# Optimization experiments

Measured on AMD Instinct MI355X. Metric: run time of the kernel, lower is better.

## Reference

```python
import jax, jax.numpy as jnp
import numpy as np

B, S, E = 2, 2048, 1024
D_ATTN, H = 1024, 16
HD = D_ATTN // H
SCALE = 1.0 / np.sqrt(D_ATTN)
ROPE_BASE = 10000.0


def setup_inputs() -> dict:
    key = jax.random.key(0)
    ks = jax.random.split(key, 7)
    def w(k, shape, scale):
        return jax.random.normal(k, shape, dtype=jnp.float32) * scale
    return {
        "q": w(ks[0], (B, S, E), 1.0),
        "k": w(ks[1], (B, S, E), 1.0),
        "v": w(ks[2], (B, S, E), 1.0),
        "Wq": w(ks[3], (D_ATTN, E), E ** -0.5),
        "Wk": w(ks[4], (D_ATTN, E), E ** -0.5),
        "Wv": w(ks[5], (D_ATTN, E), E ** -0.5),
        "Wo": w(ks[6], (E, D_ATTN), D_ATTN ** -0.5),
    }


def _rope(x):
    # x: [B, H, S, HD]; interleaved-pair rotary embedding over the seq axis
    s, d = x.shape[2], x.shape[3]
    half = d // 2
    inv_freq = 1.0 / (ROPE_BASE ** (jnp.arange(half, dtype=jnp.float32) * 2.0 / d))
    ang = jnp.arange(s, dtype=jnp.float32)[:, None] * inv_freq[None, :]  # [S, half]
    cos, sin = jnp.cos(ang), jnp.sin(ang)
    xr = x.reshape(x.shape[:-1] + (half, 2))
    x0, x1 = xr[..., 0], xr[..., 1]
    o0 = x0 * cos - x1 * sin
    o1 = x0 * sin + x1 * cos
    return jnp.stack([o0, o1], axis=-1).reshape(x.shape)


def reference(q, k, v, Wq, Wk, Wv, Wo):
    # linear projections (nn.Linear with weight [out, in]): y = x @ W^T
    qh = (q @ Wq.T).reshape(B, S, H, HD).transpose(0, 2, 1, 3)  # [B,H,S,HD]
    kh = (k @ Wk.T).reshape(B, S, H, HD).transpose(0, 2, 1, 3)
    vh = (v @ Wv.T).reshape(B, S, H, HD).transpose(0, 2, 1, 3)
    qh = _rope(qh)
    kh = _rope(kh)
    # shifted-causal mask: disallow j >= i (diagonal masked), except (0,0) allowed
    i = jnp.arange(S)[:, None]
    j = jnp.arange(S)[None, :]
    masked = j >= i                              # triu incl. diagonal
    masked = masked.at[0, 0].set(False)          # keep (0,0) so row 0 isn't all -inf
    scores = jnp.einsum("bhsd,bhtd->bhst", qh, kh) * SCALE
    scores = jnp.where(masked, -jnp.inf, scores)
    probs = jax.nn.softmax(scores, axis=-1)      # dropout omitted (eval mode)
    ctx = jnp.einsum("bhst,bhtd->bhsd", probs, vh)
    ctx = ctx.transpose(0, 2, 1, 3).reshape(B, S, D_ATTN)
    return ctx @ Wo.T
```

## Files before the change

### kernel.cpp

```cpp
#include <hip/hip_runtime.h>
#include <hip/hip_bf16.h>

#define BATCH 2
#define SEQ   2048
#define EMB   1024
#define DATTN 1024
#define NH    16
#define HD    64
#define MM    (BATCH*SEQ)
#define SCALE 0.03125f
#define MINIT -1.0e30f
#define ROPE_COEF 0.41524101186f

using bf16x8 = __attribute__((ext_vector_type(8))) short;
using f32x4  = __attribute__((ext_vector_type(4))) float;

__device__ inline short f2bf(float x) {
    __hip_bfloat16 b = __float2bfloat16(x);
    return *reinterpret_cast<short*>(&b);
}

__device__ inline void gl_lds16(const short* g, short* l) {
    __builtin_amdgcn_global_load_lds(
        (const __attribute__((address_space(1))) unsigned int*)g,
        (__attribute__((address_space(3))) unsigned int*)l, 16, 0, 0);
}

__global__ __launch_bounds__(256)
void cvt_all(const float* __restrict__ q, const float* __restrict__ k,
             const float* __restrict__ v,
             const float* __restrict__ Wq, const float* __restrict__ Wk,
             const float* __restrict__ Wv, const float* __restrict__ Wo,
             short* __restrict__ dst)
{
    const long QKV = (long)MM * EMB;
    const long WSZ = (long)DATTN * EMB;
    const long i = ((long)blockIdx.x * 256 + threadIdx.x) * 4;
    const float* s;
    long off;
    if (i < 3 * QKV) {
        const int seg = (int)(i / QKV);
        off = i - (long)seg * QKV;
        s = (seg == 0) ? q : (seg == 1) ? k : v;
    } else {
        const long j = i - 3 * QKV;
        const int seg = (int)(j / WSZ);
        off = j - (long)seg * WSZ;
        s = (seg == 0) ? Wq : (seg == 1) ? Wk : (seg == 2) ? Wv : Wo;
    }
    float4 x = *(const float4*)(s + off);
    short4 y;
    y.x = f2bf(x.x); y.y = f2bf(x.y); y.z = f2bf(x.z); y.w = f2bf(x.w);
    *(short4*)(dst + i) = y;
}

__device__ inline void stage_tile64(const short* g, short* lds, int tid) {
    #pragma unroll
    for (int c = 0; c < 4; ++c) {
        const int cc   = c * 256 + tid;
        const int row  = cc >> 3;
        const int slot = cc & 7;
        const int ssl  = slot ^ (row & 7);
        gl_lds16(g + (long)row * EMB + ssl * 8, lds + ((cc & ~63) << 3));
    }
}

__device__ inline void stage_tile64h(const short* g, short* lds, int tid) {
    #pragma unroll
    for (int c = 0; c < 2; ++c) {
        const int cc   = c * 256 + tid;
        const int row  = cc >> 3;
        const int ssl  = (cc & 7) ^ (row & 7);
        gl_lds16(g + (long)row * EMB + ssl * 8, lds + ((cc & ~63) << 3));
    }
}

__global__ __launch_bounds__(256)
void gemm_proj_bf16(const short* __restrict__ qb, const short* __restrict__ kb,
                    const short* __restrict__ vb,
                    const short* __restrict__ wqb, const short* __restrict__ wkb,
                    const short* __restrict__ wvb,
                    short* __restrict__ Qb, short* __restrict__ Kb,
                    short* __restrict__ Vtb)
{
    const short* A; const short* B;
    if (blockIdx.z == 0)      { A = qb; B = wqb; }
    else if (blockIdx.z == 1) { A = kb; B = wkb; }
    else                      { A = vb; B = wvb; }
    const bool isv = (blockIdx.z == 2);

    __shared__ short sA[128 * 64];
    __shared__ short sB[128 * 64];

    const int tid  = threadIdx.x;
    const int wave = tid >> 6, lane = tid & 63;
    const int quad = lane >> 4, l16 = lane & 15;
    const int wm = (wave >> 1) * 64, wn = (wave & 1) * 64;
    const long m0 = (long)blockIdx.x * 128, n0 = (long)blockIdx.y * 128;
    const int rsw = l16 & 7;

    f32x4 acc[4][4];
    #pragma unroll
    for (int i = 0; i < 4; ++i)
        #pragma unroll
        for (int j = 0; j < 4; ++j) acc[i][j] = (f32x4){0.f, 0.f, 0.f, 0.f};

    for (int kt = 0; kt < EMB; kt += 64) {
        __syncthreads();
        stage_tile64(A + m0 * EMB + kt, sA, tid);
        stage_tile64(B + n0 * EMB + kt, sB, tid);
        __syncthreads();

        #pragma unroll
        for (int kk = 0; kk < 2; ++kk) {
            bf16x8 af[4], bfr[4];
            #pragma unroll
            for (int rt = 0; rt < 4; ++rt)
                af[rt] = *(const bf16x8*)&sA[(wm + rt * 16 + l16) * 64
                         + (((kk << 2) | quad) ^ rsw) * 8];
            #pragma unroll
            for (int ct = 0; ct < 4; ++ct)
                bfr[ct] = *(const bf16x8*)&sB[(wn + ct * 16 + l16) * 64
                          + (((kk << 2) | quad) ^ rsw) * 8];
            if (isv) {
                #pragma unroll
                for (int i = 0; i < 4; ++i)
                    #pragma unroll
                    for (int j = 0; j < 4; ++j)
                        acc[i][j] = __builtin_amdgcn_mfma_f32_16x16x32_bf16(
                            af[i], bfr[j], acc[i][j], 0, 0, 0);
            } else {
                #pragma unroll
                for (int i = 0; i < 4; ++i)
                    #pragma unroll
                    for (int j = 0; j < 4; ++j)
                        acc[i][j] = __builtin_amdgcn_mfma_f32_16x16x32_bf16(
                            bfr[i], af[j], acc[i][j], 0, 0, 0);
            }
        }
    }

    if (!isv) {
        short* C = (blockIdx.z == 0) ? Qb : Kb;
        const float scl = (blockIdx.z == 0) ? SCALE : 1.0f;
        #pragma unroll
        for (int i = 0; i < 4; ++i) {
            const int d0  = (int)(n0) + wn + i * 16 + quad * 4;
            const int hh  = d0 >> 6, dd0 = d0 & (HD - 1);
            const float invf0 = exp2f(-ROPE_COEF * (float)(dd0 >> 1));
            const float invf1 = exp2f(-ROPE_COEF * (float)((dd0 >> 1) + 1));
            #pragma unroll
            for (int j = 0; j < 4; ++j) {
                const int tok = (int)(m0) + wm + j * 16 + l16;
                const int bb = tok >> 11, ss = tok & (SEQ - 1);
                float s0, c0, s1, c1;
                __sincosf((float)ss * invf0, &s0, &c0);
                __sincosf((float)ss * invf1, &s1, &c1);
                const f32x4 x = acc[i][j];
                short4 o4;
                o4.x = f2bf((x[0] * c0 - x[1] * s0) * scl);
                o4.y = f2bf((x[0] * s0 + x[1] * c0) * scl);
                o4.z = f2bf((x[2] * c1 - x[3] * s1) * scl);
                o4.w = f2bf((x[2] * s1 + x[3] * c1) * scl);
                *(short4*)&C[(((long)(bb * NH + hh)) << 17)
                             + ((long)ss << 6) + dd0] = o4;
            }
        }
    } else {
        #pragma unroll
        for (int rt = 0; rt < 4; ++rt) {
            #pragma unroll
            for (int ct = 0; ct < 4; ++ct) {
                const long row0 = m0 + wm + rt * 16 + quad * 4;
                const long col  = n0 + wn + ct * 16 + l16;
                const int bb = (int)(row0 >> 11), ss = (int)(row0 & (SEQ - 1));
                const int hh = (int)(col >> 6),   dd = (int)(col & (HD - 1));
                short4 s4;
                s4.x = f2bf(acc[rt][ct][0]); s4.y = f2bf(acc[rt][ct][1]);
                s4.z = f2bf(acc[rt][ct][2]); s4.w = f2bf(acc[rt][ct][3]);
                *(short4*)&Vtb[(((long)(bb * NH + hh)) << 17) + ((long)dd << 11) + ss] = s4;
            }
        }
    }
}

__global__ __launch_bounds__(256)
void gemm_out_bf16(const short* __restrict__ Ab, const short* __restrict__ Bb,
                   float* __restrict__ C)
{
    __shared__ short sA[128 * 64];
    __shared__ short sB[64 * 64];

    const int tid  = threadIdx.x;
    const int wave = tid >> 6, lane = tid & 63;
    const int quad = lane >> 4, l16 = lane & 15;
    const int wm = (wave >> 1) * 64, wn = (wave & 1) * 32;
    const long m0 = (long)blockIdx.x * 128, n0 = (long)blockIdx.y * 64;
    const int rsw = l16 & 7;

    f32x4 acc[4][2];
    #pragma unroll
    for (int i = 0; i < 4; ++i)
        #pragma unroll
        for (int j = 0; j < 2; ++j) acc[i][j] = (f32x4){0.f, 0.f, 0.f, 0.f};

    for (int kt = 0; kt < DATTN; kt += 64) {
        __syncthreads();
        stage_tile64(Ab + m0 * DATTN + kt, sA, tid);
        stage_tile64h(Bb + n0 * DATTN + kt, sB, tid);
        __syncthreads();

        #pragma unroll
        for (int kk = 0; kk < 2; ++kk) {
            bf16x8 af[4], bfr[2];
            #pragma unroll
            for (int rt = 0; rt < 4; ++rt)
                af[rt] = *(const bf16x8*)&sA[(wm + rt * 16 + l16) * 64
                         + (((kk << 2) | quad) ^ rsw) * 8];
            #pragma unroll
            for (int ct = 0; ct < 2; ++ct)
                bfr[ct] = *(const bf16x8*)&sB[(wn + ct * 16 + l16) * 64
                          + (((kk << 2) | quad) ^ rsw) * 8];
            #pragma unroll
            for (int rt = 0; rt < 4; ++rt)
                #pragma unroll
                for (int ct = 0; ct < 2; ++ct)
                    acc[rt][ct] = __builtin_amdgcn_mfma_f32_16x16x32_bf16(
                        af[rt], bfr[ct], acc[rt][ct], 0, 0, 0);
        }
    }

    #pragma unroll
    for (int rt = 0; rt < 4; ++rt) {
        #pragma unroll
        for (int ct = 0; ct < 2; ++ct) {
            #pragma unroll
            for (int reg = 0; reg < 4; ++reg) {
                const long row = m0 + wm + rt * 16 + quad * 4 + reg;
                const long col = n0 + wn + ct * 16 + l16;
                C[row * EMB + col] = acc[rt][ct][reg];
            }
        }
    }
}

#define KLD 64
#define PLD 72

__device__ inline void stage_kv64(const short* __restrict__ Kb,
                                  const short* __restrict__ Vtb,
                                  long base, int jb2,
                                  short* skp, short* svp,
                                  int tid, int wave)
{
    #pragma unroll
    for (int c = 0; c < 2; ++c) {
        const int cc  = c * 256 + tid;
        const int row = cc >> 3;
        const int sch = (cc & 7) ^ (row & 7);
        short* dk = skp + ((c * 256 + (tid & ~63)) << 3) - ((tid & ~63) << 3)
                        + (((c * 256 + tid) & ~63) - (c * 256 + tid - (tid & 63)) ) ;
        (void)dk;
        gl_lds16(Kb + base + (long)(jb2 + row) * HD + sch * 8,
                 skp + ((c * 256 + wave * 64) << 3));
        gl_lds16(Vtb + base + ((long)row << 11) + jb2 + sch * 8,
                 svp + ((c * 256 + wave * 64) << 3));
    }
}

__global__ __launch_bounds__(256, 3)
void flash_attn_mfma(const short* __restrict__ Qb,
                     const short* __restrict__ Kb,
                     const short* __restrict__ Vtb,
                     short* __restrict__ ctx)
{
    const int id  = blockIdx.x;
    const int hi  = id >> 8;
    const int idx = id & 255;
    const int r   = idx & 7;
    const int s5  = idx >> 3;
    const int pi  = s5 & 3;
    const int ts8 = s5 >> 2;
    const int p   = r + 8 * pi;
    const int b   = p >> 4, h = p & 15;
    const int t   = hi ? ts8 : (15 - ts8);

    const int tid = threadIdx.x;
    const int wave = tid >> 6, lane = tid & 63;
    const int quad = lane >> 4, l16 = lane & 15;
    const int r0 = t * 128;

    __shared__ short sk[2][64 * KLD];
    __shared__ short sv[2][64 * KLD];
    __shared__ short sp[4][32 * PLD];

    const long base = ((long)(b * NH + h)) << 17;

    const int iq0 = r0 + wave * 32 + l16;
    const int iq1 = iq0 + 16;
    const int dtile = 2 * t + (wave >> 1);
    const int rsw = l16 & 7;

    bf16x8 qf0[2], qf1[2];
    #pragma unroll
    for (int tt = 0; tt < 2; ++tt) {
        qf0[tt] = *(const bf16x8*)(Qb + base + (long)iq0 * HD + tt * 32 + quad * 8);
        qf1[tt] = *(const bf16x8*)(Qb + base + (long)iq1 * HD + tt * 32 + quad * 8);
    }

    f32x4 acc0[4], acc1[4];
    #pragma unroll
    for (int ct = 0; ct < 4; ++ct) {
        acc0[ct] = (f32x4){0.f, 0.f, 0.f, 0.f};
        acc1[ct] = (f32x4){0.f, 0.f, 0.f, 0.f};
    }
    float m0 = MINIT, l0 = 0.f;
    float m1 = MINIT, l1 = 0.f;

    const int J = 2 * t + 2;

    stage_kv64(Kb, Vtb, base, 0, sk[0], sv[0], tid, wave);

    #pragma unroll 1
    for (int j2 = 0; j2 < J; ++j2) {
        const int pb = j2 & 1;
        asm volatile("s_waitcnt vmcnt(0)" ::: "memory");
        __builtin_amdgcn_s_barrier();
        if (j2 + 1 < J)
            stage_kv64(Kb, Vtb, base, (j2 + 1) * 64,
                       sk[pb ^ 1], sv[pb ^ 1], tid, wave);

        if (j2 <= dtile) {
            const int jb2 = j2 * 64;
            const short* skh = sk[pb];
            const short* svh = sv[pb];

            f32x4 s0[4], s1[4];
            __builtin_amdgcn_s_setprio(1);
            #pragma unroll
            for (int ct = 0; ct < 4; ++ct) {
                const int rr16 = (ct * 16 + l16) * KLD;
                bf16x8 k0 = *(const bf16x8*)&skh[rr16 + ((quad ^ rsw) << 3)];
                bf16x8 k1 = *(const bf16x8*)&skh[rr16 + (((4 + quad) ^ rsw) << 3)];
                f32x4 z0 = (f32x4){0.f, 0.f, 0.f, 0.f};
                z0 = __builtin_amdgcn_mfma_f32_16x16x32_bf16(k0, qf0[0], z0, 0, 0, 0);
                z0 = __builtin_amdgcn_mfma_f32_16x16x32_bf16(k1, qf0[1], z0, 0, 0, 0);
                s0[ct] = z0;
                f32x4 z1 = (f32x4){0.f, 0.f, 0.f, 0.f};
                z1 = __builtin_amdgcn_mfma_f32_16x16x32_bf16(k0, qf1[0], z1, 0, 0, 0);
                z1 = __builtin_amdgcn_mfma_f32_16x16x32_bf16(k1, qf1[1], z1, 0, 0, 0);
                s1[ct] = z1;
            }
            __builtin_amdgcn_s_setprio(0);

            if (j2 == dtile) {
                #pragma unroll
                for (int ct = 0; ct < 4; ++ct)
                    #pragma unroll
                    for (int rr = 0; rr < 4; ++rr) {
                        const int j = jb2 + ct * 16 + quad * 4 + rr;
                        if (!((j < iq0) || (iq0 == 0 && j == 0)))
                            s0[ct][rr] = -INFINITY;
                        if (!(j < iq1))
                            s1[ct][rr] = -INFINITY;
                    }
            }

            float mx0 = MINIT;
            #pragma unroll
            for (int ct = 0; ct < 4; ++ct)
                #pragma unroll
                for (int rr = 0; rr < 4; ++rr) mx0 = fmaxf(mx0, s0[ct][rr]);
            mx0 = fmaxf(mx0, __shfl_xor(mx0, 16, 64));
            mx0 = fmaxf(mx0, __shfl_xor(mx0, 32, 64));
            const float mn0 = fmaxf(m0, mx0);
            const float a0 = __expf(m0 - mn0);
            m0 = mn0;
            float ss0 = 0.f;
            #pragma unroll
            for (int ct = 0; ct < 4; ++ct)
                #pragma unroll
                for (int rr = 0; rr < 4; ++rr) {
                    const float e = __expf(s0[ct][rr] - mn0);
                    s0[ct][rr] = e;
                    ss0 += e;
                }
            ss0 += __shfl_xor(ss0, 16, 64);
            ss0 += __shfl_xor(ss0, 32, 64);
            l0 = l0 * a0 + ss0;

            float mx1 = MINIT;
            #pragma unroll
            for (int ct = 0; ct < 4; ++ct)
                #pragma unroll
                for (int rr = 0; rr < 4; ++rr) mx1 = fmaxf(mx1, s1[ct][rr]);
            mx1 = fmaxf(mx1, __shfl_xor(mx1, 16, 64));
            mx1 = fmaxf(mx1, __shfl_xor(mx1, 32, 64));
            const float mn1 = fmaxf(m1, mx1);
            const float a1 = __expf(m1 - mn1);
            m1 = mn1;
            float ss1 = 0.f;
            #pragma unroll
            for (int ct = 0; ct < 4; ++ct)
                #pragma unroll
                for (int rr = 0; rr < 4; ++rr) {
                    const float e = __expf(s1[ct][rr] - mn1);
                    s1[ct][rr] = e;
                    ss1 += e;
                }
            ss1 += __shfl_xor(ss1, 16, 64);
            ss1 += __shfl_xor(ss1, 32, 64);
            l1 = l1 * a1 + ss1;

            short* pw0 = sp[wave];
            short* pw1 = sp[wave] + 16 * PLD;
            #pragma unroll
            for (int ct = 0; ct < 4; ++ct) {
                short4 p4;
                p4.x = f2bf(s0[ct][0]); p4.y = f2bf(s0[ct][1]);
                p4.z = f2bf(s0[ct][2]); p4.w = f2bf(s0[ct][3]);
                *(short4*)&pw0[l16 * PLD + ct * 16 + quad * 4] = p4;
                short4 q4;
                q4.x = f2bf(s1[ct][0]); q4.y = f2bf(s1[ct][1]);
                q4.z = f2bf(s1[ct][2]); q4.w = f2bf(s1[ct][3]);
                *(short4*)&pw1[l16 * PLD + ct * 16 + quad * 4] = q4;
            }

            #pragma unroll
            for (int ct = 0; ct < 4; ++ct)
                #pragma unroll
                for (int rr = 0; rr < 4; ++rr) {
                    acc0[ct][rr] *= a0;
                    acc1[ct][rr] *= a1;
                }

            bf16x8 pf00 = *(const bf16x8*)&pw0[l16 * PLD + quad * 8];
            bf16x8 pf01 = *(const bf16x8*)&pw0[l16 * PLD + 32 + quad * 8];
            bf16x8 pf10 = *(const bf16x8*)&pw1[l16 * PLD + quad * 8];
            bf16x8 pf11 = *(const bf16x8*)&pw1[l16 * PLD + 32 + quad * 8];

            __builtin_amdgcn_s_setprio(1);
            #pragma unroll
            for (int ct = 0; ct < 4; ++ct) {
                const int rr16 = (ct * 16 + l16) * KLD;
                bf16x8 v0 = *(const bf16x8*)&svh[rr16 + ((quad ^ rsw) << 3)];
                bf16x8 v1 = *(const bf16x8*)&svh[rr16 + (((4 + quad) ^ rsw) << 3)];
                acc0[ct] = __builtin_amdgcn_mfma_f32_16x16x32_bf16(
                    v0, pf00, acc0[ct], 0, 0, 0);
                acc0[ct] = __builtin_amdgcn_mfma_f32_16x16x32_bf16(
                    v1, pf01, acc0[ct], 0, 0, 0);
                acc1[ct] = __builtin_amdgcn_mfma_f32_16x16x32_bf16(
                    v0, pf10, acc1[ct], 0, 0, 0);
                acc1[ct] = __builtin_amdgcn_mfma_f32_16x16x32_bf16(
                    v1, pf11, acc1[ct], 0, 0, 0);
            }
            __builtin_amdgcn_s_setprio(0);
        }
    }

    {
        const float inv0 = 1.f / l0;
        short* orow = ctx + (long)(b * SEQ + iq0) * DATTN + h * HD;
        #pragma unroll
        for (int ct = 0; ct < 4; ++ct) {
            short4 o4;
            o4.x = f2bf(acc0[ct][0] * inv0);
            o4.y = f2bf(acc0[ct][1] * inv0);
            o4.z = f2bf(acc0[ct][2] * inv0);
            o4.w = f2bf(acc0[ct][3] * inv0);
            *(short4*)&orow[ct * 16 + quad * 4] = o4;
        }
    }
    {
        const float inv1 = 1.f / l1;
        short* orow = ctx + (long)(b * SEQ + iq1) * DATTN + h * HD;
        #pragma unroll
        for (int ct = 0; ct < 4; ++ct) {
            short4 o4;
            o4.x = f2bf(acc1[ct][0] * inv1);
            o4.y = f2bf(acc1[ct][1] * inv1);
            o4.z = f2bf(acc1[ct][2] * inv1);
            o4.w = f2bf(acc1[ct][3] * inv1);
            *(short4*)&orow[ct * 16 + quad * 4] = o4;
        }
    }
}

extern "C" void kernel_launch(void* const* d_in, const int* in_sizes, int n_in,
                              void* d_out, int out_size, void* d_ws, size_t ws_size,
                              hipStream_t stream) {
    const float* q  = (const float*)d_in[0];
    const float* k  = (const float*)d_in[1];
    const float* v  = (const float*)d_in[2];
    const float* Wq = (const float*)d_in[3];
    const float* Wk = (const float*)d_in[4];
    const float* Wv = (const float*)d_in[5];
    const float* Wo = (const float*)d_in[6];
    float* out = (float*)d_out;

    const long QKV = (long)MM * EMB;
    const long WSZ = (long)DATTN * EMB;
    short* basep = (short*)d_ws;
    short* qb  = basep;
    short* kb  = qb + QKV;
    short* vb  = kb + QKV;
    short* wqb = vb + QKV;
    short* wkb = wqb + WSZ;
    short* wvb = wkb + WSZ;
    short* wob = wvb + WSZ;
    short* Qb  = wob + WSZ;
    short* Kb  = Qb + QKV;
    short* Vtb = Kb + QKV;
    short* ctx = Vtb + QKV;

    cvt_all<<<16384, 256, 0, stream>>>(q, k, v, Wq, Wk, Wv, Wo, qb);

    gemm_proj_bf16<<<dim3(MM / 128, DATTN / 128, 3), 256, 0, stream>>>(
        qb, kb, vb, wqb, wkb, wvb, Qb, Kb, Vtb);

    flash_attn_mfma<<<512, 256, 0, stream>>>(Qb, Kb, Vtb, ctx);

    gemm_out_bf16<<<dim3(MM / 128, EMB / 64), 256, 0, stream>>>(ctx, wob, out);
}
```

Before: 211.0 us.

## Fold log2e into Q scale, skip rescale when max unchanged, double-buffer out GEMM

Q is pre-scaled by SCALE*log2(e) so softmax can use exp2f directly. Accumulator and row-sum rescaling is skipped when no lane's running max grew. The output projection GEMM gets double-buffered LDS tiles with a prefetch of the next K slice, cutting one barrier per iteration. The changes add wave-uniform branches and double the output GEMM's LDS footprint.

After: 221.8 us. 1.05x slower.

```diff
diff --git a/kernel.cpp b/kernel.cpp
--- a/kernel.cpp
+++ b/kernel.cpp
@@ -9,6 +9,7 @@
 #define HD    64
 #define MM    (BATCH*SEQ)
 #define SCALE 0.03125f
+#define QSCALE 0.0450842200278f
 #define MINIT -1.0e30f
 #define ROPE_COEF 0.41524101186f
 
@@ -142,7 +143,7 @@
 
     if (!isv) {
         short* C = (blockIdx.z == 0) ? Qb : Kb;
-        const float scl = (blockIdx.z == 0) ? SCALE : 1.0f;
+        const float scl = (blockIdx.z == 0) ? QSCALE : 1.0f;
         #pragma unroll
         for (int i = 0; i < 4; ++i) {
             const int d0  = (int)(n0) + wn + i * 16 + quad * 4;
@@ -188,8 +189,8 @@
 void gemm_out_bf16(const short* __restrict__ Ab, const short* __restrict__ Bb,
                    float* __restrict__ C)
 {
-    __shared__ short sA[128 * 64];
-    __shared__ short sB[64 * 64];
+    __shared__ short sA[2][128 * 64];
+    __shared__ short sB[2][64 * 64];
 
     const int tid  = threadIdx.x;
     const int wave = tid >> 6, lane = tid & 63;
@@ -204,22 +205,29 @@
         #pragma unroll
         for (int j = 0; j < 2; ++j) acc[i][j] = (f32x4){0.f, 0.f, 0.f, 0.f};
 
-    for (int kt = 0; kt < DATTN; kt += 64) {
-        __syncthreads();
-        stage_tile64(Ab + m0 * DATTN + kt, sA, tid);
-        stage_tile64h(Bb + n0 * DATTN + kt, sB, tid);
-        __syncthreads();
+    stage_tile64(Ab + m0 * DATTN, sA[0], tid);
+    stage_tile64h(Bb + n0 * DATTN, sB[0], tid);
+
+    #pragma unroll 1
+    for (int s = 0; s < 16; ++s) {
+        const int pb = s & 1;
+        asm volatile("s_waitcnt vmcnt(0)" ::: "memory");
+        __builtin_amdgcn_s_barrier();
+        if (s + 1 < 16) {
+            stage_tile64(Ab + m0 * DATTN + (s + 1) * 64, sA[pb ^ 1], tid);
+            stage_tile64h(Bb + n0 * DATTN + (s + 1) * 64, sB[pb ^ 1], tid);
+        }
 
         #pragma unroll
         for (int kk = 0; kk < 2; ++kk) {
             bf16x8 af[4], bfr[2];
             #pragma unroll
             for (int rt = 0; rt < 4; ++rt)
-                af[rt] = *(const bf16x8*)&sA[(wm + rt * 16 + l16) * 64
+                af[rt] = *(const bf16x8*)&sA[pb][(wm + rt * 16 + l16) * 64
                          + (((kk << 2) | quad) ^ rsw) * 8];
             #pragma unroll
             for (int ct = 0; ct < 2; ++ct)
-                bfr[ct] = *(const bf16x8*)&sB[(wn + ct * 16 + l16) * 64
+                bfr[ct] = *(const bf16x8*)&sB[pb][(wn + ct * 16 + l16) * 64
                           + (((kk << 2) | quad) ^ rsw) * 8];
             #pragma unroll
             for (int rt = 0; rt < 4; ++rt)
@@ -258,9 +266,6 @@
         const int cc  = c * 256 + tid;
         const int row = cc >> 3;
         const int sch = (cc & 7) ^ (row & 7);
-        short* dk = skp + ((c * 256 + (tid & ~63)) << 3) - ((tid & ~63) << 3)
-                        + (((c * 256 + tid) & ~63) - (c * 256 + tid - (tid & 63)) ) ;
-        (void)dk;
         gl_lds16(Kb + base + (long)(jb2 + row) * HD + sch * 8,
                  skp + ((c * 256 + wave * 64) << 3));
         gl_lds16(Vtb + base + ((long)row << 11) + jb2 + sch * 8,
@@ -373,21 +378,21 @@
                 for (int rr = 0; rr < 4; ++rr) mx0 = fmaxf(mx0, s0[ct][rr]);
             mx0 = fmaxf(mx0, __shfl_xor(mx0, 16, 64));
             mx0 = fmaxf(mx0, __shfl_xor(mx0, 32, 64));
-            const float mn0 = fmaxf(m0, mx0);
-            const float a0 = __expf(m0 - mn0);
+            const float mo0 = m0;
+            const float mn0 = fmaxf(mo0, mx0);
             m0 = mn0;
             float ss0 = 0.f;
             #pragma unroll
             for (int ct = 0; ct < 4; ++ct)
                 #pragma unroll
                 for (int rr = 0; rr < 4; ++rr) {
-                    const float e = __expf(s0[ct][rr] - mn0);
+                    const float e = exp2f(s0[ct][rr] - mn0);
                     s0[ct][rr] = e;
                     ss0 += e;
                 }
             ss0 += __shfl_xor(ss0, 16, 64);
             ss0 += __shfl_xor(ss0, 32, 64);
-            l0 = l0 * a0 + ss0;
+            const bool grow0 = __any(mx0 > mo0);
 
             float mx1 = MINIT;
             #pragma unroll
@@ -396,21 +401,21 @@
                 for (int rr = 0; rr < 4; ++rr) mx1 = fmaxf(mx1, s1[ct][rr]);
             mx1 = fmaxf(mx1, __shfl_xor(mx1, 16, 64));
             mx1 = fmaxf(mx1, __shfl_xor(mx1, 32, 64));
-            const float mn1 = fmaxf(m1, mx1);
-            const float a1 = __expf(m1 - mn1);
+            const float mo1 = m1;
+            const float mn1 = fmaxf(mo1, mx1);
             m1 = mn1;
             float ss1 = 0.f;
             #pragma unroll
             for (int ct = 0; ct < 4; ++ct)
                 #pragma unroll
                 for (int rr = 0; rr < 4; ++rr) {
-                    const float e = __expf(s1[ct][rr] - mn1);
+                    const float e = exp2f(s1[ct][rr] - mn1);
                     s1[ct][rr] = e;
                     ss1 += e;
                 }
             ss1 += __shfl_xor(ss1, 16, 64);
             ss1 += __shfl_xor(ss1, 32, 64);
-            l1 = l1 * a1 + ss1;
+            const bool grow1 = __any(mx1 > mo1);
 
             short* pw0 = sp[wave];
             short* pw1 = sp[wave] + 16 * PLD;
@@ -426,13 +431,26 @@
                 *(short4*)&pw1[l16 * PLD + ct * 16 + quad * 4] = q4;
             }
 
-            #pragma unroll
-            for (int ct = 0; ct < 4; ++ct)
-                #pragma unroll
-                for (int rr = 0; rr < 4; ++rr) {
-                    acc0[ct][rr] *= a0;
-                    acc1[ct][rr] *= a1;
-                }
+            if (grow0) {
+                const float a0 = exp2f(mo0 - mn0);
+                #pragma unroll
+                for (int ct = 0; ct < 4; ++ct)
+                    #pragma unroll
+                    for (int rr = 0; rr < 4; ++rr) acc0[ct][rr] *= a0;
+                l0 = l0 * a0 + ss0;
+            } else {
+                l0 += ss0;
+            }
+            if (grow1) {
+                const float a1 = exp2f(mo1 - mn1);
+                #pragma unroll
+                for (int ct = 0; ct < 4; ++ct)
+                    #pragma unroll
+                    for (int rr = 0; rr < 4; ++rr) acc1[ct][rr] *= a1;
+                l1 = l1 * a1 + ss1;
+            } else {
+                l1 += ss1;
+            }
 
             bf16x8 pf00 = *(const bf16x8*)&pw0[l16 * PLD + quad * 8];
             bf16x8 pf01 = *(const bf16x8*)&pw0[l16 * PLD + 32 + quad * 8];
```
